# Kernel tuning notes

Hardware: AMD Instinct MI355X
Metric: run time of the kernel (lower is better)

## Reference

```python
import jax, jax.numpy as jnp
import numpy as np

DIM = 1024
HEADS = 8
DIM_HEAD = 64
INNER = HEADS * DIM_HEAD
SCALE = DIM_HEAD ** -0.5


def setup_inputs() -> dict:
    key = jax.random.key(0)
    ks = jax.random.split(key, 6)
    b, n = 2, 2048
    x = jax.random.normal(ks[0], (b, n, DIM), dtype=jnp.float32)
    rel_pos_bias = jax.random.normal(ks[1], (HEADS, n, n), dtype=jnp.float32)
    # learned params (Linear stores W as [out, in]; we keep [in, out] for x @ W)
    Wq = jax.random.normal(ks[2], (DIM, INNER), dtype=jnp.float32) * (DIM ** -0.5)
    Wkv = jax.random.normal(ks[3], (DIM, 2 * DIM_HEAD), dtype=jnp.float32) * (DIM ** -0.5)
    Wo = jax.random.normal(ks[4], (INNER, DIM), dtype=jnp.float32) * (INNER ** -0.5)
    bo = jax.random.normal(ks[5], (DIM,), dtype=jnp.float32) * 0.01
    return {"x": x, "rel_pos_bias": rel_pos_bias, "Wq": Wq, "Wkv": Wkv, "Wo": Wo, "bo": bo}


def reference(x, rel_pos_bias, Wq, Wkv, Wo, bo):
    b, n, _ = x.shape
    q = x @ Wq                       # [b, n, h*d]
    kv = x @ Wkv                     # [b, n, 2d] (multi-query: single shared kv head)
    k, v = kv[..., :DIM_HEAD], kv[..., DIM_HEAD:]
    q = q.reshape(b, n, HEADS, DIM_HEAD).transpose(0, 2, 1, 3) * SCALE  # [b, h, n, d]
    sim = jnp.einsum('bhid,bjd->bhij', q, k)
    sim = sim + rel_pos_bias         # bias broadcast over batch
    causal_mask = jnp.triu(jnp.ones((n, n), dtype=bool), k=1)
    neg = -jnp.finfo(sim.dtype).max
    sim = jnp.where(causal_mask, neg, sim)
    attn = jax.nn.softmax(sim, axis=-1)  # stable softmax (max-subtract internally)
    out = jnp.einsum('bhij,bjd->bhid', attn, v)
    out = out.transpose(0, 2, 1, 3).reshape(b, n, INNER)  # [b, n, h*d]
    return out @ Wo + bo
```

## Files before the change

kernel.cpp:

```cpp
#include <hip/hip_runtime.h>

#define NSEQ 2048
#define NB 2
#define NH 8
#define HD 64
#define DMODEL 1024
#define DINNER 512

#define SLOT_F 4224
#define LOG2E 1.44269504f

typedef __attribute__((ext_vector_type(8))) short bf16x8;
typedef __attribute__((ext_vector_type(4))) float f32x4;

__device__ __forceinline__ ushort f2bf(float f) {
  uint u = __float_as_uint(f);
  uint r = (u + 0x7fffu + ((u >> 16) & 1u)) >> 16;
  return (ushort)r;
}

__device__ __forceinline__ void gld16(const ushort* g, ushort* l) {
  __builtin_amdgcn_global_load_lds(
      (const __attribute__((address_space(1))) uint*)g,
      (__attribute__((address_space(3))) uint*)l, 16, 0, 0);
}

__global__ __launch_bounds__(256) void cast_x_kernel(
    const float* __restrict__ x, ushort* __restrict__ xb) {
  size_t i = ((size_t)blockIdx.x * 256 + threadIdx.x) * 8;
  float4 a = *(const float4*)(x + i);
  float4 b = *(const float4*)(x + i + 4);
  ushort4 o1, o2;
  o1.x = f2bf(a.x); o1.y = f2bf(a.y); o1.z = f2bf(a.z); o1.w = f2bf(a.w);
  o2.x = f2bf(b.x); o2.y = f2bf(b.y); o2.z = f2bf(b.z); o2.w = f2bf(b.w);
  *(ushort4*)(xb + i) = o1;
  *(ushort4*)(xb + i + 4) = o2;
}

__global__ __launch_bounds__(256) void transpose_cast_kernel(
    const float* __restrict__ srcA, const float* __restrict__ srcB,
    int ldA, int ldB, int nsplit, int Ktot, ushort* __restrict__ dst) {
  __shared__ float t[64][65];
  const int k0 = blockIdx.x * 64;
  const int n0 = blockIdx.y * 64;
  const float* src; int ld, nb;
  if (n0 < nsplit) { src = srcA; ld = ldA; nb = n0; }
  else { src = srcB; ld = ldB; nb = n0 - nsplit; }
  const int r = threadIdx.x >> 4;
  const int c = (threadIdx.x & 15) * 4;
#pragma unroll
  for (int rr = r; rr < 64; rr += 16) {
    float4 v = *(const float4*)(src + (size_t)(k0 + rr) * ld + nb + c);
    t[rr][c + 0] = v.x; t[rr][c + 1] = v.y; t[rr][c + 2] = v.z; t[rr][c + 3] = v.w;
  }
  __syncthreads();
#pragma unroll
  for (int rr = r; rr < 64; rr += 16) {
    ushort4 o;
    o.x = f2bf(t[c + 0][rr]); o.y = f2bf(t[c + 1][rr]);
    o.z = f2bf(t[c + 2][rr]); o.w = f2bf(t[c + 3][rr]);
    *(ushort4*)(dst + (size_t)(n0 + rr) * Ktot + k0 + c) = o;
  }
}

__device__ __forceinline__ void stage_tile(const ushort* __restrict__ src, int ld,
                                           int row0, int k0, ushort* lds, int tid) {
#pragma unroll
  for (int i = 0; i < 4; ++i) {
    const int cix = i * 256 + tid;
    const int row = cix >> 3, j = cix & 7;
    uint4 v = *(const uint4*)(src + (size_t)(row0 + row) * ld + k0 + j * 8);
    *(uint4*)((char*)lds + row * 128 + ((j ^ (row & 7)) << 4)) = v;
  }
}

__device__ __forceinline__ void gemm_tile(const ushort* __restrict__ A,
                                          const ushort* __restrict__ Bt, int K,
                                          int m0, int n0, ushort* As, ushort* Bs,
                                          int tid, f32x4 acc[4][4]) {
  const int lane = tid & 63;
  const int w = tid >> 6;
  const int wr = w >> 1, wc = w & 1;
  const int lr = lane & 15, lg = lane >> 4;
  for (int k0 = 0; k0 < K; k0 += 64) {
    __syncthreads();
    stage_tile(A, K, m0, k0, As, tid);
    stage_tile(Bt, K, n0, k0, Bs, tid);
    __syncthreads();
#pragma unroll
    for (int kk = 0; kk < 2; ++kk) {
      bf16x8 af[4], bfr[4];
#pragma unroll
      for (int mi = 0; mi < 4; ++mi) {
        const int r = wr * 64 + mi * 16 + lr;
        af[mi] = *(const bf16x8*)((char*)As + r * 128 + (((kk * 4 + lg) ^ (r & 7)) << 4));
      }
#pragma unroll
      for (int ni = 0; ni < 4; ++ni) {
        const int r = wc * 64 + ni * 16 + lr;
        bfr[ni] = *(const bf16x8*)((char*)Bs + r * 128 + (((kk * 4 + lg) ^ (r & 7)) << 4));
      }
#pragma unroll
      for (int mi = 0; mi < 4; ++mi)
#pragma unroll
        for (int ni = 0; ni < 4; ++ni)
          acc[mi][ni] = __builtin_amdgcn_mfma_f32_16x16x32_bf16(af[mi], bfr[ni],
                                                                acc[mi][ni], 0, 0, 0);
    }
  }
}

__global__ __launch_bounds__(256) void qkv_mfma_kernel(
    const ushort* __restrict__ xb, const ushort* __restrict__ WT1,
    ushort* __restrict__ qb, ushort* __restrict__ ksw, ushort* __restrict__ vsw) {
  __shared__ ushort As[128 * 64];
  __shared__ ushort Bs[128 * 64];
  const int tid = threadIdx.x;
  const int m0 = blockIdx.x * 128, n0 = blockIdx.y * 128;
  f32x4 acc[4][4];
#pragma unroll
  for (int a = 0; a < 4; ++a)
#pragma unroll
    for (int b = 0; b < 4; ++b) acc[a][b] = (f32x4){0.f, 0.f, 0.f, 0.f};
  gemm_tile(xb, WT1, DMODEL, m0, n0, As, Bs, tid, acc);
  const int lane = tid & 63;
  const int w = tid >> 6;
  const int wr = w >> 1, wc = w & 1;
  const int lr = lane & 15, lg = lane >> 4;
#pragma unroll
  for (int mi = 0; mi < 4; ++mi)
#pragma unroll
    for (int ni = 0; ni < 4; ++ni) {
      const int n = n0 + wc * 64 + ni * 16 + lr;
      if (n >= 640) continue;
#pragma unroll
      for (int r = 0; r < 4; ++r) {
        const int m = m0 + wr * 64 + mi * 16 + lg * 4 + r;
        const int bb = m >> 11, key = m & (NSEQ - 1);
        const float v = acc[mi][ni][r];
        if (n < DINNER) {
          const int h = n >> 6, d = n & 63;
          qb[((size_t)((bb * NH + h) * NSEQ) + key) * HD + d] =
              f2bf(v * (0.125f * LOG2E));
        } else if (n < DINNER + HD) {
          const int d = n - DINNER;
          const int t = key >> 6, row = key & 63;
          const int ch = d >> 3, pos = d & 7;
          ksw[(size_t)((bb * 32 + t) * 64 + row) * 64 +
              ((ch ^ (row & 7)) << 3) + pos] = f2bf(v);
        } else {
          const int d = n - DINNER - HD;
          const int pr = key >> 7, kk = key & 127;
          const int ch = kk >> 3, pos = kk & 7;
          vsw[(size_t)((bb * 16 + pr) * 64 + d) * 128 +
              ((ch ^ (d & 15)) << 3) + pos] = f2bf(v);
        }
      }
    }
}

__global__ __launch_bounds__(256) void out_mfma_kernel(
    const ushort* __restrict__ ab, const ushort* __restrict__ WoT,
    const float* __restrict__ bo, float* __restrict__ out) {
  __shared__ ushort As[128 * 64];
  __shared__ ushort Bs[128 * 64];
  const int tid = threadIdx.x;
  const int m0 = blockIdx.x * 128, n0 = blockIdx.y * 128;
  f32x4 acc[4][4];
#pragma unroll
  for (int a = 0; a < 4; ++a)
#pragma unroll
    for (int b = 0; b < 4; ++b) acc[a][b] = (f32x4){0.f, 0.f, 0.f, 0.f};
  gemm_tile(ab, WoT, DINNER, m0, n0, As, Bs, tid, acc);
  const int lane = tid & 63;
  const int w = tid >> 6;
  const int wr = w >> 1, wc = w & 1;
  const int lr = lane & 15, lg = lane >> 4;
#pragma unroll
  for (int mi = 0; mi < 4; ++mi)
#pragma unroll
    for (int ni = 0; ni < 4; ++ni) {
      const int n = n0 + wc * 64 + ni * 16 + lr;
      const float bias = bo[n];
#pragma unroll
      for (int r = 0; r < 4; ++r) {
        const int m = m0 + wr * 64 + mi * 16 + lg * 4 + r;
        out[(size_t)m * DMODEL + n] = acc[mi][ni][r] + bias;
      }
    }
}

__global__ __launch_bounds__(256) void attn_mfma_kernel(
    const ushort* __restrict__ qb, const ushort* __restrict__ ksw,
    const ushort* __restrict__ vsw, const float* __restrict__ rpb,
    ushort* __restrict__ ob, float* __restrict__ scratch) {
  __shared__ ushort Ks[2 * 128 * 64];
  __shared__ ushort Vs[2 * 64 * 128];
  __shared__ ushort Ps[4 * 16 * 128];
  const int tid = threadIdx.x;
  const int lane = tid & 63;
  const int w = tid >> 6;
  const int id = blockIdx.x;
  const int bh = id & 15;
  int qt, p0, p1, partial, ch;
  if (id < 256) {
    qt = 16 + (id >> 4); ch = 0; p0 = 0; p1 = 8; partial = 1;
  } else if (id < 512) {
    qt = 31 - ((id - 256) >> 4); ch = 1; p0 = 8; p1 = (qt >> 1) + 1; partial = 1;
  } else {
    qt = 15 - ((id - 512) >> 4); ch = 0; p0 = 0; p1 = (qt >> 1) + 1; partial = 0;
  }
  const int bb = bh >> 3, h = bh & 7;
  const int q0 = qt * 64;
  const int lr = lane & 15;
  const int lg = lane >> 4;
  const int pdiag = qt >> 1;
  const int qg = q0 + w * 16 + lr;

  const ushort* kpair = ksw + (size_t)bb * 32 * 64 * 64;
  const ushort* vpair = vsw + (size_t)bb * 16 * 64 * 128;
  const ushort* ksrcw = kpair + w * 2048 + lane * 8;
  const ushort* vsrcw = vpair + w * 2048 + lane * 8;
  ushort* kdstw = Ks + w * 2048;
  ushort* vdstw = Vs + w * 2048;

#define ISSUE(pp, bsel)                                                     \
  {                                                                         \
    const ushort* _ks = ksrcw + (size_t)(pp) * 8192;                        \
    const ushort* _vs = vsrcw + (size_t)(pp) * 8192;                        \
    ushort* _kd = kdstw + (bsel) * 8192;                                    \
    ushort* _vd = vdstw + (bsel) * 8192;                                    \
    gld16(_ks + 0 * 512, _kd + 0 * 512);                                    \
    gld16(_ks + 1 * 512, _kd + 1 * 512);                                    \
    gld16(_ks + 2 * 512, _kd + 2 * 512);                                    \
    gld16(_ks + 3 * 512, _kd + 3 * 512);                                    \
    gld16(_vs + 0 * 512, _vd + 0 * 512);                                    \
    gld16(_vs + 1 * 512, _vd + 1 * 512);                                    \
    gld16(_vs + 2 * 512, _vd + 2 * 512);                                    \
    gld16(_vs + 3 * 512, _vd + 3 * 512);                                    \
  }

#define LOAD_BIAS(pp, dst)                                                  \
  {                                                                         \
    const float* _br = rpb + (size_t)h * NSEQ * NSEQ +                      \
                       (size_t)qg * NSEQ + (pp) * 128 + lg * 4;             \
    _Pragma("unroll")                                                       \
    for (int _ct = 0; _ct < 8; ++_ct)                                       \
      dst[_ct] = *(const f32x4*)(_br + _ct * 16);                           \
  }

  bf16x8 qf[2];
  {
    const ushort* qrow = qb + ((size_t)(bh * NSEQ) + qg) * HD + lg * 8;
    qf[0] = *(const bf16x8*)qrow;
    qf[1] = *(const bf16x8*)(qrow + 32);
  }
  f32x4 oaccT[4];
#pragma unroll
  for (int dt = 0; dt < 4; ++dt) oaccT[dt] = (f32x4){0.f, 0.f, 0.f, 0.f};
  float m_run = -1e30f, l_run = 0.f;

  f32x4 bias_c[8], bias_n[8];

  ISSUE(p0, 0);
  LOAD_BIAS(p0, bias_c);
  ISSUE(p0 + 1, 1);
  int curb = 0;

  for (int p = p0; p < p1; ++p) {
    if (p < p1 - 1) {
      asm volatile("s_waitcnt vmcnt(16)" ::: "memory");
    } else {
      asm volatile("s_waitcnt vmcnt(8)" ::: "memory");
    }
    __builtin_amdgcn_sched_barrier(0);
    __builtin_amdgcn_s_barrier();

    const char* Kc = (const char*)(Ks + curb * 8192);
    const char* Vc = (const char*)(Vs + curb * 8192);
    f32x4 s[8];
    __builtin_amdgcn_s_setprio(1);
#pragma unroll
    for (int ct = 0; ct < 8; ++ct) {
      s[ct] = (f32x4){0.f, 0.f, 0.f, 0.f};
      const int krow = ct * 16 + lr;
#pragma unroll
      for (int kk = 0; kk < 2; ++kk) {
        bf16x8 kf = *(const bf16x8*)(Kc + krow * 128 +
                                     (((kk * 4 + lg) ^ (krow & 7)) << 4));
        s[ct] = __builtin_amdgcn_mfma_f32_16x16x32_bf16(kf, qf[kk], s[ct], 0, 0, 0);
      }
    }
    __builtin_amdgcn_s_setprio(0);
    if (p + 1 < p1) LOAD_BIAS(p + 1, bias_n);
#pragma unroll
    for (int ct = 0; ct < 8; ++ct)
#pragma unroll
      for (int r = 0; r < 4; ++r)
        s[ct][r] = fmaf(bias_c[ct][r], LOG2E, s[ct][r]);
    if (p == pdiag) {
#pragma unroll
      for (int ct = 0; ct < 8; ++ct) {
        const int kg = p * 128 + ct * 16 + lg * 4;
#pragma unroll
        for (int r = 0; r < 4; ++r)
          if (kg + r > qg) s[ct][r] = -1e30f;
      }
    }
    float cm[8];
#pragma unroll
    for (int ct = 0; ct < 8; ++ct)
      cm[ct] = fmaxf(fmaxf(s[ct][0], s[ct][1]), fmaxf(s[ct][2], s[ct][3]));
    float mt = fmaxf(fmaxf(fmaxf(cm[0], cm[1]), fmaxf(cm[2], cm[3])),
                     fmaxf(fmaxf(cm[4], cm[5]), fmaxf(cm[6], cm[7])));
    mt = fmaxf(mt, __shfl_xor(mt, 16, 64));
    mt = fmaxf(mt, __shfl_xor(mt, 32, 64));
    const float m_new = fmaxf(m_run, mt);
    const float fac = exp2f(m_run - m_new);
    m_run = m_new;
    float cs[8];
#pragma unroll
    for (int ct = 0; ct < 8; ++ct) {
#pragma unroll
      for (int r = 0; r < 4; ++r) s[ct][r] = exp2f(s[ct][r] - m_new);
      cs[ct] = (s[ct][0] + s[ct][1]) + (s[ct][2] + s[ct][3]);
    }
    float ls = ((cs[0] + cs[1]) + (cs[2] + cs[3])) +
               ((cs[4] + cs[5]) + (cs[6] + cs[7]));
    ls += __shfl_xor(ls, 16, 64);
    ls += __shfl_xor(ls, 32, 64);
    l_run = l_run * fac + ls;
#pragma unroll
    for (int dt = 0; dt < 4; ++dt) oaccT[dt] *= fac;
    char* Pw = (char*)Ps + w * 4096;
#pragma unroll
    for (int ct = 0; ct < 8; ++ct) {
      uint u01, u23;
      asm("v_cvt_pk_bf16_f32 %0, %1, %2" : "=v"(u01) : "v"(s[ct][0]), "v"(s[ct][1]));
      asm("v_cvt_pk_bf16_f32 %0, %1, %2" : "=v"(u23) : "v"(s[ct][2]), "v"(s[ct][3]));
      const int chunk = 2 * ct + (lg >> 1);
      uint2 uv; uv.x = u01; uv.y = u23;
      *(uint2*)(Pw + lr * 256 + (((chunk ^ lr) << 4) | ((lg & 1) * 8))) = uv;
    }
    __builtin_amdgcn_s_setprio(1);
#pragma unroll
    for (int kk = 0; kk < 4; ++kk) {
      bf16x8 pf = *(const bf16x8*)(Pw + lr * 256 + (((kk * 4 + lg) ^ lr) << 4));
#pragma unroll
      for (int dt = 0; dt < 4; ++dt) {
        const int vrow = dt * 16 + lr;
        bf16x8 vf = *(const bf16x8*)(Vc + vrow * 256 +
                                     (((kk * 4 + lg) ^ (vrow & 15)) << 4));
        oaccT[dt] =
            __builtin_amdgcn_mfma_f32_16x16x32_bf16(vf, pf, oaccT[dt], 0, 0, 0);
      }
    }
    __builtin_amdgcn_s_setprio(0);
    __builtin_amdgcn_sched_barrier(0);
    __builtin_amdgcn_s_barrier();
    if (p + 2 < p1) ISSUE(p + 2, curb);
    if (p + 1 < p1) {
#pragma unroll
      for (int ct = 0; ct < 8; ++ct) bias_c[ct] = bias_n[ct];
    }
    curb ^= 1;
  }
#undef ISSUE
#undef LOAD_BIAS
  if (!partial) {
    const float inv = 1.0f / l_run;
    ushort* dst = ob + ((size_t)(bb * NSEQ) + qg) * DINNER + h * HD;
#pragma unroll
    for (int dt = 0; dt < 4; ++dt) {
      uint u01, u23;
      const float o0 = oaccT[dt][0] * inv, o1 = oaccT[dt][1] * inv;
      const float o2 = oaccT[dt][2] * inv, o3 = oaccT[dt][3] * inv;
      asm("v_cvt_pk_bf16_f32 %0, %1, %2" : "=v"(u01) : "v"(o0), "v"(o1));
      asm("v_cvt_pk_bf16_f32 %0, %1, %2" : "=v"(u23) : "v"(o2), "v"(o3));
      uint2 uv; uv.x = u01; uv.y = u23;
      *(uint2*)(dst + dt * 16 + lg * 4) = uv;
    }
  } else {
    float* slot = scratch + (size_t)((bh * 16 + (qt - 16)) * 2 + ch) * SLOT_F;
    const int row = w * 16 + lr;
#pragma unroll
    for (int dt = 0; dt < 4; ++dt)
      *(f32x4*)(slot + row * 64 + dt * 16 + lg * 4) = oaccT[dt];
    if (lg == 0) {
      slot[4096 + row] = m_run;
      slot[4160 + row] = l_run;
    }
  }
}

__global__ __launch_bounds__(256) void attn_merge_kernel(
    const float* __restrict__ scratch, ushort* __restrict__ ob) {
  const int bid = blockIdx.x;
  const int bh = bid >> 4;
  const int qt = 16 + (bid & 15);
  const int bb = bh >> 3, h = bh & 7;
  const float* s0 = scratch + (size_t)((bh * 16 + (qt - 16)) * 2) * SLOT_F;
  const float* s1 = s0 + SLOT_F;
  const int t = threadIdx.x;
  const int r = t >> 2;
  const int c0 = (t & 3) * 16;
  const float m0 = s0[4096 + r], m1 = s1[4096 + r];
  const float M = fmaxf(m0, m1);
  const float sc0 = exp2f(m0 - M), sc1 = exp2f(m1 - M);
  const float L = s0[4160 + r] * sc0 + s1[4160 + r] * sc1;
  const float inv = 1.0f / L;
  ushort* dst = ob + ((size_t)(bb * NSEQ) + qt * 64 + r) * DINNER + h * HD + c0;
#pragma unroll
  for (int j4 = 0; j4 < 4; ++j4) {
    float4 a = *(const float4*)(s0 + r * 64 + c0 + j4 * 4);
    float4 b = *(const float4*)(s1 + r * 64 + c0 + j4 * 4);
    dst[j4 * 4 + 0] = f2bf((a.x * sc0 + b.x * sc1) * inv);
    dst[j4 * 4 + 1] = f2bf((a.y * sc0 + b.y * sc1) * inv);
    dst[j4 * 4 + 2] = f2bf((a.z * sc0 + b.z * sc1) * inv);
    dst[j4 * 4 + 3] = f2bf((a.w * sc0 + b.w * sc1) * inv);
  }
}

extern "C" void kernel_launch(void* const* d_in, const int* in_sizes, int n_in,
                              void* d_out, int out_size, void* d_ws, size_t ws_size,
                              hipStream_t stream) {
  (void)in_sizes; (void)n_in; (void)out_size; (void)ws_size;
  const float* x = (const float*)d_in[0];
  const float* rpb = (const float*)d_in[1];
  const float* Wq = (const float*)d_in[2];
  const float* Wkv = (const float*)d_in[3];
  const float* Wo = (const float*)d_in[4];
  const float* bo = (const float*)d_in[5];
  float* out = (float*)d_out;

  ushort* qbb = (ushort*)d_ws;
  ushort* ksw = qbb + (size_t)NB * NH * NSEQ * HD;
  ushort* vsw = ksw + (size_t)NB * NSEQ * HD;
  ushort* obuf = vsw + (size_t)NB * NSEQ * HD;
  ushort* xb = obuf + (size_t)NB * NSEQ * DINNER;
  ushort* WT1 = xb + (size_t)NB * NSEQ * DMODEL;
  ushort* WoT = WT1 + (size_t)640 * DMODEL;
  float* scratch = (float*)(WoT + (size_t)DMODEL * DINNER);

  cast_x_kernel<<<dim3(2048), 256, 0, stream>>>(x, xb);
  transpose_cast_kernel<<<dim3(16, 10), 256, 0, stream>>>(Wq, Wkv, 512, 128, 512,
                                                          DMODEL, WT1);
  transpose_cast_kernel<<<dim3(8, 16), 256, 0, stream>>>(Wo, Wo, DMODEL, DMODEL,
                                                         DMODEL, DINNER, WoT);
  qkv_mfma_kernel<<<dim3(32, 5), 256, 0, stream>>>(xb, WT1, qbb, ksw, vsw);
  attn_mfma_kernel<<<dim3(768), 256, 0, stream>>>(qbb, ksw, vsw, rpb, obuf,
                                                  scratch);
  attn_merge_kernel<<<dim3(256), 256, 0, stream>>>(scratch, obuf);
  out_mfma_kernel<<<dim3(32, 8), 256, 0, stream>>>(obuf, WoT, bo, out);
}
```

Before: 98.97 us.

## Split attention into single-wave blocks with finer key chunks and direct global K/V reads

New measurement: 163.1 us. +64.8%, slower.

```diff
diff --git a/kernel.cpp b/kernel.cpp
--- a/kernel.cpp
+++ b/kernel.cpp
@@ -7,7 +7,7 @@
 #define DMODEL 1024
 #define DINNER 512
 
-#define SLOT_F 4224
+#define SLOT_F 1056
 #define LOG2E 1.44269504f
 
 typedef __attribute__((ext_vector_type(8))) short bf16x8;
@@ -19,10 +19,10 @@
   return (ushort)r;
 }
 
-__device__ __forceinline__ void gld16(const ushort* g, ushort* l) {
-  __builtin_amdgcn_global_load_lds(
-      (const __attribute__((address_space(1))) uint*)g,
-      (__attribute__((address_space(3))) uint*)l, 16, 0, 0);
+__device__ __forceinline__ int soff(int s, int c) {
+  if (s < 64) return (s - 32) * 2 + c;
+  if (s < 96) return 64 + (s - 64) * 3 + c;
+  return 160 + (s - 96) * 4 + c;
 }
 
 __global__ __launch_bounds__(256) void cast_x_kernel(
@@ -112,7 +112,7 @@
 
 __global__ __launch_bounds__(256) void qkv_mfma_kernel(
     const ushort* __restrict__ xb, const ushort* __restrict__ WT1,
-    ushort* __restrict__ qb, ushort* __restrict__ ksw, ushort* __restrict__ vsw) {
+    ushort* __restrict__ qb, ushort* __restrict__ kb, ushort* __restrict__ vt) {
   __shared__ ushort As[128 * 64];
   __shared__ ushort Bs[128 * 64];
   const int tid = threadIdx.x;
@@ -143,17 +143,9 @@
           qb[((size_t)((bb * NH + h) * NSEQ) + key) * HD + d] =
               f2bf(v * (0.125f * LOG2E));
         } else if (n < DINNER + HD) {
-          const int d = n - DINNER;
-          const int t = key >> 6, row = key & 63;
-          const int ch = d >> 3, pos = d & 7;
-          ksw[(size_t)((bb * 32 + t) * 64 + row) * 64 +
-              ((ch ^ (row & 7)) << 3) + pos] = f2bf(v);
+          kb[((size_t)(bb * NSEQ) + key) * HD + (n - DINNER)] = f2bf(v);
         } else {
-          const int d = n - DINNER - HD;
-          const int pr = key >> 7, kk = key & 127;
-          const int ch = kk >> 3, pos = kk & 7;
-          vsw[(size_t)((bb * 16 + pr) * 64 + d) * 128 +
-              ((ch ^ (d & 15)) << 3) + pos] = f2bf(v);
+          vt[((size_t)(bb * HD) + (n - DINNER - HD)) * NSEQ + key] = f2bf(v);
         }
       }
     }
@@ -190,64 +182,31 @@
     }
 }
 
-__global__ __launch_bounds__(256) void attn_mfma_kernel(
-    const ushort* __restrict__ qb, const ushort* __restrict__ ksw,
-    const ushort* __restrict__ vsw, const float* __restrict__ rpb,
+__global__ __launch_bounds__(64, 3) void attn_mfma_kernel(
+    const ushort* __restrict__ qb, const ushort* __restrict__ kb,
+    const ushort* __restrict__ vt, const float* __restrict__ rpb,
     ushort* __restrict__ ob, float* __restrict__ scratch) {
-  __shared__ ushort Ks[2 * 128 * 64];
-  __shared__ ushort Vs[2 * 64 * 128];
-  __shared__ ushort Ps[4 * 16 * 128];
-  const int tid = threadIdx.x;
-  const int lane = tid & 63;
-  const int w = tid >> 6;
+  __shared__ ushort Ps[16 * 128];
+  const int lane = threadIdx.x;
+  const int lr = lane & 15;
+  const int lg = lane >> 4;
   const int id = blockIdx.x;
   const int bh = id & 15;
-  int qt, p0, p1, partial, ch;
-  if (id < 256) {
-    qt = 16 + (id >> 4); ch = 0; p0 = 0; p1 = 8; partial = 1;
-  } else if (id < 512) {
-    qt = 31 - ((id - 256) >> 4); ch = 1; p0 = 8; p1 = (qt >> 1) + 1; partial = 1;
-  } else {
-    qt = 15 - ((id - 512) >> 4); ch = 0; p0 = 0; p1 = (qt >> 1) + 1; partial = 0;
-  }
+  const int t = 319 - (id >> 4);
+  int s, c;
+  if (t < 32)       { s = t;                      c = 0; }
+  else if (t < 96)  { int u = t - 32;  s = 32 + (u >> 1); c = u & 1; }
+  else if (t < 192) { int u = t - 96;  s = 64 + u / 3;    c = u % 3; }
+  else              { int u = t - 192; s = 96 + (u >> 2); c = u & 3; }
   const int bb = bh >> 3, h = bh & 7;
-  const int q0 = qt * 64;
-  const int lr = lane & 15;
-  const int lg = lane >> 4;
-  const int pdiag = qt >> 1;
-  const int qg = q0 + w * 16 + lr;
-
-  const ushort* kpair = ksw + (size_t)bb * 32 * 64 * 64;
-  const ushort* vpair = vsw + (size_t)bb * 16 * 64 * 128;
-  const ushort* ksrcw = kpair + w * 2048 + lane * 8;
-  const ushort* vsrcw = vpair + w * 2048 + lane * 8;
-  ushort* kdstw = Ks + w * 2048;
-  ushort* vdstw = Vs + w * 2048;
-
-#define ISSUE(pp, bsel)                                                     \
-  {                                                                         \
-    const ushort* _ks = ksrcw + (size_t)(pp) * 8192;                        \
-    const ushort* _vs = vsrcw + (size_t)(pp) * 8192;                        \
-    ushort* _kd = kdstw + (bsel) * 8192;                                    \
-    ushort* _vd = vdstw + (bsel) * 8192;                                    \
-    gld16(_ks + 0 * 512, _kd + 0 * 512);                                    \
-    gld16(_ks + 1 * 512, _kd + 1 * 512);                                    \
-    gld16(_ks + 2 * 512, _kd + 2 * 512);                                    \
-    gld16(_ks + 3 * 512, _kd + 3 * 512);                                    \
-    gld16(_vs + 0 * 512, _vd + 0 * 512);                                    \
-    gld16(_vs + 1 * 512, _vd + 1 * 512);                                    \
-    gld16(_vs + 2 * 512, _vd + 2 * 512);                                    \
-    gld16(_vs + 3 * 512, _vd + 3 * 512);                                    \
-  }
-
-#define LOAD_BIAS(pp, dst)                                                  \
-  {                                                                         \
-    const float* _br = rpb + (size_t)h * NSEQ * NSEQ +                      \
-                       (size_t)qg * NSEQ + (pp) * 128 + lg * 4;             \
-    _Pragma("unroll")                                                       \
-    for (int _ct = 0; _ct < 8; ++_ct)                                       \
-      dst[_ct] = *(const f32x4*)(_br + _ct * 16);                           \
-  }
+  const int pdiag = s >> 3;
+  const int p0 = c * 4;
+  const int p1 = min(p0 + 4, pdiag + 1);
+  const int nch = (pdiag + 4) >> 2;
+  const int qg = s * 16 + lr;
+
+  const ushort* kbase = kb + (size_t)bb * NSEQ * HD;
+  const ushort* vbase = vt + (size_t)bb * HD * NSEQ;
 
   bf16x8 qf[2];
   {
@@ -260,57 +219,46 @@
   for (int dt = 0; dt < 4; ++dt) oaccT[dt] = (f32x4){0.f, 0.f, 0.f, 0.f};
   float m_run = -1e30f, l_run = 0.f;
 
-  f32x4 bias_c[8], bias_n[8];
-
-  ISSUE(p0, 0);
-  LOAD_BIAS(p0, bias_c);
-  ISSUE(p0 + 1, 1);
-  int curb = 0;
-
   for (int p = p0; p < p1; ++p) {
-    if (p < p1 - 1) {
-      asm volatile("s_waitcnt vmcnt(16)" ::: "memory");
-    } else {
-      asm volatile("s_waitcnt vmcnt(8)" ::: "memory");
-    }
-    __builtin_amdgcn_sched_barrier(0);
-    __builtin_amdgcn_s_barrier();
-
-    const char* Kc = (const char*)(Ks + curb * 8192);
-    const char* Vc = (const char*)(Vs + curb * 8192);
-    f32x4 s[8];
+    const int key0 = p * 128;
+    f32x4 bias[8];
+    {
+      const float* br =
+          rpb + (size_t)h * NSEQ * NSEQ + (size_t)qg * NSEQ + key0 + lg * 4;
+#pragma unroll
+      for (int ct = 0; ct < 8; ++ct) bias[ct] = *(const f32x4*)(br + ct * 16);
+    }
+    f32x4 sv[8];
     __builtin_amdgcn_s_setprio(1);
 #pragma unroll
     for (int ct = 0; ct < 8; ++ct) {
-      s[ct] = (f32x4){0.f, 0.f, 0.f, 0.f};
-      const int krow = ct * 16 + lr;
-#pragma unroll
-      for (int kk = 0; kk < 2; ++kk) {
-        bf16x8 kf = *(const bf16x8*)(Kc + krow * 128 +
-                                     (((kk * 4 + lg) ^ (krow & 7)) << 4));
-        s[ct] = __builtin_amdgcn_mfma_f32_16x16x32_bf16(kf, qf[kk], s[ct], 0, 0, 0);
-      }
+      const ushort* krow =
+          kbase + (size_t)(key0 + ct * 16 + lr) * HD + lg * 8;
+      bf16x8 kf0 = *(const bf16x8*)krow;
+      bf16x8 kf1 = *(const bf16x8*)(krow + 32);
+      sv[ct] = (f32x4){0.f, 0.f, 0.f, 0.f};
+      sv[ct] = __builtin_amdgcn_mfma_f32_16x16x32_bf16(kf0, qf[0], sv[ct], 0, 0, 0);
+      sv[ct] = __builtin_amdgcn_mfma_f32_16x16x32_bf16(kf1, qf[1], sv[ct], 0, 0, 0);
     }
     __builtin_amdgcn_s_setprio(0);
-    if (p + 1 < p1) LOAD_BIAS(p + 1, bias_n);
 #pragma unroll
     for (int ct = 0; ct < 8; ++ct)
 #pragma unroll
       for (int r = 0; r < 4; ++r)
-        s[ct][r] = fmaf(bias_c[ct][r], LOG2E, s[ct][r]);
+        sv[ct][r] = fmaf(bias[ct][r], LOG2E, sv[ct][r]);
     if (p == pdiag) {
 #pragma unroll
       for (int ct = 0; ct < 8; ++ct) {
-        const int kg = p * 128 + ct * 16 + lg * 4;
+        const int kg = key0 + ct * 16 + lg * 4;
 #pragma unroll
         for (int r = 0; r < 4; ++r)
-          if (kg + r > qg) s[ct][r] = -1e30f;
+          if (kg + r > qg) sv[ct][r] = -1e30f;
       }
     }
     float cm[8];
 #pragma unroll
     for (int ct = 0; ct < 8; ++ct)
-      cm[ct] = fmaxf(fmaxf(s[ct][0], s[ct][1]), fmaxf(s[ct][2], s[ct][3]));
+      cm[ct] = fmaxf(fmaxf(sv[ct][0], sv[ct][1]), fmaxf(sv[ct][2], sv[ct][3]));
     float mt = fmaxf(fmaxf(fmaxf(cm[0], cm[1]), fmaxf(cm[2], cm[3])),
                      fmaxf(fmaxf(cm[4], cm[5]), fmaxf(cm[6], cm[7])));
     mt = fmaxf(mt, __shfl_xor(mt, 16, 64));
@@ -322,8 +270,8 @@
 #pragma unroll
     for (int ct = 0; ct < 8; ++ct) {
 #pragma unroll
-      for (int r = 0; r < 4; ++r) s[ct][r] = exp2f(s[ct][r] - m_new);
-      cs[ct] = (s[ct][0] + s[ct][1]) + (s[ct][2] + s[ct][3]);
+      for (int r = 0; r < 4; ++r) sv[ct][r] = exp2f(sv[ct][r] - m_new);
+      cs[ct] = (sv[ct][0] + sv[ct][1]) + (sv[ct][2] + sv[ct][3]);
     }
     float ls = ((cs[0] + cs[1]) + (cs[2] + cs[3])) +
                ((cs[4] + cs[5]) + (cs[6] + cs[7]));
@@ -332,12 +280,12 @@
     l_run = l_run * fac + ls;
 #pragma unroll
     for (int dt = 0; dt < 4; ++dt) oaccT[dt] *= fac;
-    char* Pw = (char*)Ps + w * 4096;
+    char* Pw = (char*)Ps;
 #pragma unroll
     for (int ct = 0; ct < 8; ++ct) {
       uint u01, u23;
-      asm("v_cvt_pk_bf16_f32 %0, %1, %2" : "=v"(u01) : "v"(s[ct][0]), "v"(s[ct][1]));
-      asm("v_cvt_pk_bf16_f32 %0, %1, %2" : "=v"(u23) : "v"(s[ct][2]), "v"(s[ct][3]));
+      asm("v_cvt_pk_bf16_f32 %0, %1, %2" : "=v"(u01) : "v"(sv[ct][0]), "v"(sv[ct][1]));
+      asm("v_cvt_pk_bf16_f32 %0, %1, %2" : "=v"(u23) : "v"(sv[ct][2]), "v"(sv[ct][3]));
       const int chunk = 2 * ct + (lg >> 1);
       uint2 uv; uv.x = u01; uv.y = u23;
       *(uint2*)(Pw + lr * 256 + (((chunk ^ lr) << 4) | ((lg & 1) * 8))) = uv;
@@ -348,26 +296,16 @@
       bf16x8 pf = *(const bf16x8*)(Pw + lr * 256 + (((kk * 4 + lg) ^ lr) << 4));
 #pragma unroll
       for (int dt = 0; dt < 4; ++dt) {
-        const int vrow = dt * 16 + lr;
-        bf16x8 vf = *(const bf16x8*)(Vc + vrow * 256 +
-                                     (((kk * 4 + lg) ^ (vrow & 15)) << 4));
+        const ushort* vrow =
+            vbase + (size_t)(dt * 16 + lr) * NSEQ + key0 + kk * 32 + lg * 8;
+        bf16x8 vf = *(const bf16x8*)vrow;
         oaccT[dt] =
             __builtin_amdgcn_mfma_f32_16x16x32_bf16(vf, pf, oaccT[dt], 0, 0, 0);
       }
     }
     __builtin_amdgcn_s_setprio(0);
-    __builtin_amdgcn_sched_barrier(0);
-    __builtin_amdgcn_s_barrier();
-    if (p + 2 < p1) ISSUE(p + 2, curb);
-    if (p + 1 < p1) {
-#pragma unroll
-      for (int ct = 0; ct < 8; ++ct) bias_c[ct] = bias_n[ct];
-    }
-    curb ^= 1;
-  }
-#undef ISSUE
-#undef LOAD_BIAS
-  if (!partial) {
+  }
+  if (nch == 1) {
     const float inv = 1.0f / l_run;
     ushort* dst = ob + ((size_t)(bb * NSEQ) + qg) * DINNER + h * HD;
 #pragma unroll
@@ -381,44 +319,58 @@
       *(uint2*)(dst + dt * 16 + lg * 4) = uv;
     }
   } else {
-    float* slot = scratch + (size_t)((bh * 16 + (qt - 16)) * 2 + ch) * SLOT_F;
-    const int row = w * 16 + lr;
+    float* slot = scratch + ((size_t)(bh * 288) + soff(s, c)) * SLOT_F;
 #pragma unroll
     for (int dt = 0; dt < 4; ++dt)
-      *(f32x4*)(slot + row * 64 + dt * 16 + lg * 4) = oaccT[dt];
+      *(f32x4*)(slot + lr * 64 + dt * 16 + lg * 4) = oaccT[dt];
     if (lg == 0) {
-      slot[4096 + row] = m_run;
-      slot[4160 + row] = l_run;
-    }
-  }
-}
-
-__global__ __launch_bounds__(256) void attn_merge_kernel(
+      slot[1024 + lr] = m_run;
+      slot[1040 + lr] = l_run;
+    }
+  }
+}
+
+__global__ __launch_bounds__(64) void attn_merge_kernel(
     const float* __restrict__ scratch, ushort* __restrict__ ob) {
   const int bid = blockIdx.x;
-  const int bh = bid >> 4;
-  const int qt = 16 + (bid & 15);
+  const int bh = bid / 96;
+  const int s = 32 + bid % 96;
+  const int nch = ((s >> 3) + 4) >> 2;
   const int bb = bh >> 3, h = bh & 7;
-  const float* s0 = scratch + (size_t)((bh * 16 + (qt - 16)) * 2) * SLOT_F;
-  const float* s1 = s0 + SLOT_F;
+  const float* base = scratch + ((size_t)(bh * 288) + soff(s, 0)) * SLOT_F;
   const int t = threadIdx.x;
   const int r = t >> 2;
   const int c0 = (t & 3) * 16;
-  const float m0 = s0[4096 + r], m1 = s1[4096 + r];
-  const float M = fmaxf(m0, m1);
-  const float sc0 = exp2f(m0 - M), sc1 = exp2f(m1 - M);
-  const float L = s0[4160 + r] * sc0 + s1[4160 + r] * sc1;
+  float ms[4], M = -1e30f;
+  for (int ch = 0; ch < nch; ++ch) {
+    ms[ch] = base[(size_t)ch * SLOT_F + 1024 + r];
+    M = fmaxf(M, ms[ch]);
+  }
+  float L = 0.f, sc[4];
+  for (int ch = 0; ch < nch; ++ch) {
+    sc[ch] = exp2f(ms[ch] - M);
+    L += base[(size_t)ch * SLOT_F + 1040 + r] * sc[ch];
+  }
   const float inv = 1.0f / L;
-  ushort* dst = ob + ((size_t)(bb * NSEQ) + qt * 64 + r) * DINNER + h * HD + c0;
-#pragma unroll
-  for (int j4 = 0; j4 < 4; ++j4) {
-    float4 a = *(const float4*)(s0 + r * 64 + c0 + j4 * 4);
-    float4 b = *(const float4*)(s1 + r * 64 + c0 + j4 * 4);
-    dst[j4 * 4 + 0] = f2bf((a.x * sc0 + b.x * sc1) * inv);
-    dst[j4 * 4 + 1] = f2bf((a.y * sc0 + b.y * sc1) * inv);
-    dst[j4 * 4 + 2] = f2bf((a.z * sc0 + b.z * sc1) * inv);
-    dst[j4 * 4 + 3] = f2bf((a.w * sc0 + b.w * sc1) * inv);
-  }
+  float o[16];
+#pragma unroll
+  for (int j = 0; j < 16; ++j) o[j] = 0.f;
+  for (int ch = 0; ch < nch; ++ch) {
+    const float* orow = base + (size_t)ch * SLOT_F + r * 64 + c0;
+    const float f = sc[ch];
+#pragma unroll
+    for (int j4 = 0; j4 < 4; ++j4) {
+      float4 v = *(const float4*)(orow + j4 * 4);
+      o[j4 * 4 + 0] += f * v.x;
+      o[j4 * 4 + 1] += f * v.y;
+      o[j4 * 4 + 2] += f * v.z;
+      o[j4 * 4 + 3] += f * v.w;
+    }
+  }
+  ushort* dst =
+      ob + ((size_t)(bb * NSEQ) + s * 16 + r) * DINNER + h * HD + c0;
+#pragma unroll
+  for (int j = 0; j < 16; ++j) dst[j] = f2bf(o[j] * inv);
 }
 
 extern "C" void kernel_launch(void* const* d_in, const int* in_sizes, int n_in,
@@ -434,9 +386,9 @@
   float* out = (float*)d_out;
 
   ushort* qbb = (ushort*)d_ws;
-  ushort* ksw = qbb + (size_t)NB * NH * NSEQ * HD;
-  ushort* vsw = ksw + (size_t)NB * NSEQ * HD;
-  ushort* obuf = vsw + (size_t)NB * NSEQ * HD;
+  ushort* kbb = qbb + (size_t)NB * NH * NSEQ * HD;
+  ushort* vtb = kbb + (size_t)NB * NSEQ * HD;
+  ushort* obuf = vtb + (size_t)NB * NSEQ * HD;
   ushort* xb = obuf + (size_t)NB * NSEQ * DINNER;
   ushort* WT1 = xb + (size_t)NB * NSEQ * DMODEL;
   ushort* WoT = WT1 + (size_t)640 * DMODEL;
@@ -447,9 +399,9 @@
                                                           DMODEL, WT1);
   transpose_cast_kernel<<<dim3(8, 16), 256, 0, stream>>>(Wo, Wo, DMODEL, DMODEL,
                                                          DMODEL, DINNER, WoT);
-  qkv_mfma_kernel<<<dim3(32, 5), 256, 0, stream>>>(xb, WT1, qbb, ksw, vsw);
-  attn_mfma_kernel<<<dim3(768), 256, 0, stream>>>(qbb, ksw, vsw, rpb, obuf,
-                                                  scratch);
-  attn_merge_kernel<<<dim3(256), 256, 0, stream>>>(scratch, obuf);
+  qkv_mfma_kernel<<<dim3(32, 5), 256, 0, stream>>>(xb, WT1, qbb, kbb, vtb);
+  attn_mfma_kernel<<<dim3(16 * 320), 64, 0, stream>>>(qbb, kbb, vtb, rpb, obuf,
+                                                      scratch);
+  attn_merge_kernel<<<dim3(16 * 96), 64, 0, stream>>>(scratch, obuf);
   out_mfma_kernel<<<dim3(32, 8), 256, 0, stream>>>(obuf, WoT, bo, out);
 }
```

## Use 64-wide key tiles and split long query tiles into up to four KV chunks

Applied to the files above, without the earlier changes.

New measurement: 100.4 us. Within noise of the previous version (+1.4%).

```diff
diff --git a/kernel.cpp b/kernel.cpp
--- a/kernel.cpp
+++ b/kernel.cpp
@@ -8,6 +8,7 @@
 #define DINNER 512
 
 #define SLOT_F 4224
+#define SLOTS_PER_BH 72
 #define LOG2E 1.44269504f
 
 typedef __attribute__((ext_vector_type(8))) short bf16x8;
@@ -17,6 +18,12 @@
   uint u = __float_as_uint(f);
   uint r = (u + 0x7fffu + ((u >> 16) & 1u)) >> 16;
   return (ushort)r;
+}
+
+__device__ __forceinline__ int slot_off(int qt) {
+  if (qt < 16) return (qt - 8) * 2;
+  if (qt < 24) return 16 + (qt - 16) * 3;
+  return 40 + (qt - 24) * 4;
 }
 
 __device__ __forceinline__ void gld16(const ushort* g, ushort* l) {
@@ -145,15 +152,13 @@
         } else if (n < DINNER + HD) {
           const int d = n - DINNER;
           const int t = key >> 6, row = key & 63;
-          const int ch = d >> 3, pos = d & 7;
           ksw[(size_t)((bb * 32 + t) * 64 + row) * 64 +
-              ((ch ^ (row & 7)) << 3) + pos] = f2bf(v);
+              (((d >> 3) ^ (row & 7)) << 3) + (d & 7)] = f2bf(v);
         } else {
           const int d = n - DINNER - HD;
-          const int pr = key >> 7, kk = key & 127;
-          const int ch = kk >> 3, pos = kk & 7;
-          vsw[(size_t)((bb * 16 + pr) * 64 + d) * 128 +
-              ((ch ^ (d & 15)) << 3) + pos] = f2bf(v);
+          const int t = key >> 6, kk = key & 63;
+          vsw[(size_t)((bb * 32 + t) * 64 + d) * 64 +
+              (((kk >> 3) ^ (d & 7)) << 3) + (kk & 7)] = f2bf(v);
         }
       }
     }
@@ -194,58 +199,55 @@
     const ushort* __restrict__ qb, const ushort* __restrict__ ksw,
     const ushort* __restrict__ vsw, const float* __restrict__ rpb,
     ushort* __restrict__ ob, float* __restrict__ scratch) {
-  __shared__ ushort Ks[2 * 128 * 64];
-  __shared__ ushort Vs[2 * 64 * 128];
-  __shared__ ushort Ps[4 * 16 * 128];
+  __shared__ ushort Ks[2 * 64 * 64];
+  __shared__ ushort Vs[2 * 64 * 64];
+  __shared__ ushort Ps[4 * 16 * 64];
   const int tid = threadIdx.x;
   const int lane = tid & 63;
   const int w = tid >> 6;
   const int id = blockIdx.x;
   const int bh = id & 15;
-  int qt, p0, p1, partial, ch;
-  if (id < 256) {
-    qt = 16 + (id >> 4); ch = 0; p0 = 0; p1 = 8; partial = 1;
-  } else if (id < 512) {
-    qt = 31 - ((id - 256) >> 4); ch = 1; p0 = 8; p1 = (qt >> 1) + 1; partial = 1;
-  } else {
-    qt = 15 - ((id - 512) >> 4); ch = 0; p0 = 0; p1 = (qt >> 1) + 1; partial = 0;
-  }
+  const int cid = 79 - (id >> 4);
+  int qt, ch;
+  if (cid < 8)       { qt = cid;                    ch = 0; }
+  else if (cid < 24) { qt = 8 + ((cid - 8) >> 1);   ch = (cid - 8) & 1; }
+  else if (cid < 48) { qt = 16 + (cid - 24) / 3;    ch = (cid - 24) % 3; }
+  else               { qt = 24 + ((cid - 48) >> 2); ch = (cid - 48) & 3; }
+  const int t0 = ch * 8;
+  const int t1 = min(t0 + 8, qt + 1);
+  const int nit = t1 - t0;
+  const int partial = (qt >= 8);
   const int bb = bh >> 3, h = bh & 7;
   const int q0 = qt * 64;
   const int lr = lane & 15;
   const int lg = lane >> 4;
-  const int pdiag = qt >> 1;
   const int qg = q0 + w * 16 + lr;
 
-  const ushort* kpair = ksw + (size_t)bb * 32 * 64 * 64;
-  const ushort* vpair = vsw + (size_t)bb * 16 * 64 * 128;
-  const ushort* ksrcw = kpair + w * 2048 + lane * 8;
-  const ushort* vsrcw = vpair + w * 2048 + lane * 8;
-  ushort* kdstw = Ks + w * 2048;
-  ushort* vdstw = Vs + w * 2048;
-
-#define ISSUE(pp, bsel)                                                     \
+  const ushort* kbase = ksw + (size_t)bb * 32 * 4096;
+  const ushort* vbase = vsw + (size_t)bb * 32 * 4096;
+  const ushort* ksrcw = kbase + w * 1024 + lane * 8;
+  const ushort* vsrcw = vbase + w * 1024 + lane * 8;
+  ushort* kdstw = Ks + w * 1024;
+  ushort* vdstw = Vs + w * 1024;
+
+#define ISSUE(tt, bsel)                                                     \
   {                                                                         \
-    const ushort* _ks = ksrcw + (size_t)(pp) * 8192;                        \
-    const ushort* _vs = vsrcw + (size_t)(pp) * 8192;                        \
-    ushort* _kd = kdstw + (bsel) * 8192;                                    \
-    ushort* _vd = vdstw + (bsel) * 8192;                                    \
-    gld16(_ks + 0 * 512, _kd + 0 * 512);                                    \
-    gld16(_ks + 1 * 512, _kd + 1 * 512);                                    \
-    gld16(_ks + 2 * 512, _kd + 2 * 512);                                    \
-    gld16(_ks + 3 * 512, _kd + 3 * 512);                                    \
-    gld16(_vs + 0 * 512, _vd + 0 * 512);                                    \
-    gld16(_vs + 1 * 512, _vd + 1 * 512);                                    \
-    gld16(_vs + 2 * 512, _vd + 2 * 512);                                    \
-    gld16(_vs + 3 * 512, _vd + 3 * 512);                                    \
-  }
-
-#define LOAD_BIAS(pp, dst)                                                  \
+    const ushort* _ks = ksrcw + (size_t)(tt) * 4096;                        \
+    const ushort* _vs = vsrcw + (size_t)(tt) * 4096;                        \
+    ushort* _kd = kdstw + (bsel) * 4096;                                    \
+    ushort* _vd = vdstw + (bsel) * 4096;                                    \
+    gld16(_ks, _kd);                                                        \
+    gld16(_ks + 512, _kd + 512);                                            \
+    gld16(_vs, _vd);                                                        \
+    gld16(_vs + 512, _vd + 512);                                            \
+  }
+
+#define LOAD_BIAS(tt, dst)                                                  \
   {                                                                         \
     const float* _br = rpb + (size_t)h * NSEQ * NSEQ +                      \
-                       (size_t)qg * NSEQ + (pp) * 128 + lg * 4;             \
+                       (size_t)qg * NSEQ + (tt) * 64 + lg * 4;              \
     _Pragma("unroll")                                                       \
-    for (int _ct = 0; _ct < 8; ++_ct)                                       \
+    for (int _ct = 0; _ct < 4; ++_ct)                                       \
       dst[_ct] = *(const f32x4*)(_br + _ct * 16);                           \
   }
 
@@ -260,28 +262,29 @@
   for (int dt = 0; dt < 4; ++dt) oaccT[dt] = (f32x4){0.f, 0.f, 0.f, 0.f};
   float m_run = -1e30f, l_run = 0.f;
 
-  f32x4 bias_c[8], bias_n[8];
-
-  ISSUE(p0, 0);
-  LOAD_BIAS(p0, bias_c);
-  ISSUE(p0 + 1, 1);
+  f32x4 bias_c[4], bias_n[4];
+
+  ISSUE(t0, 0);
+  LOAD_BIAS(t0, bias_c);
+  ISSUE(t0 + 1, 1);
   int curb = 0;
 
-  for (int p = p0; p < p1; ++p) {
-    if (p < p1 - 1) {
-      asm volatile("s_waitcnt vmcnt(16)" ::: "memory");
+  for (int i = 0; i < nit; ++i) {
+    const int jt = t0 + i;
+    if (i < nit - 1) {
+      asm volatile("s_waitcnt vmcnt(8)" ::: "memory");
     } else {
-      asm volatile("s_waitcnt vmcnt(8)" ::: "memory");
+      asm volatile("s_waitcnt vmcnt(4)" ::: "memory");
     }
     __builtin_amdgcn_sched_barrier(0);
     __builtin_amdgcn_s_barrier();
 
-    const char* Kc = (const char*)(Ks + curb * 8192);
-    const char* Vc = (const char*)(Vs + curb * 8192);
-    f32x4 s[8];
+    const char* Kc = (const char*)(Ks + curb * 4096);
+    const char* Vc = (const char*)(Vs + curb * 4096);
+    f32x4 s[4];
     __builtin_amdgcn_s_setprio(1);
 #pragma unroll
-    for (int ct = 0; ct < 8; ++ct) {
+    for (int ct = 0; ct < 4; ++ct) {
       s[ct] = (f32x4){0.f, 0.f, 0.f, 0.f};
       const int krow = ct * 16 + lr;
 #pragma unroll
@@ -292,65 +295,64 @@
       }
     }
     __builtin_amdgcn_s_setprio(0);
-    if (p + 1 < p1) LOAD_BIAS(p + 1, bias_n);
-#pragma unroll
-    for (int ct = 0; ct < 8; ++ct)
+    if (i + 1 < nit) LOAD_BIAS(jt + 1, bias_n);
+#pragma unroll
+    for (int ct = 0; ct < 4; ++ct)
 #pragma unroll
       for (int r = 0; r < 4; ++r)
         s[ct][r] = fmaf(bias_c[ct][r], LOG2E, s[ct][r]);
-    if (p == pdiag) {
-#pragma unroll
-      for (int ct = 0; ct < 8; ++ct) {
-        const int kg = p * 128 + ct * 16 + lg * 4;
+    if (jt == qt) {
+#pragma unroll
+      for (int ct = 0; ct < 4; ++ct) {
+        const int kg = jt * 64 + ct * 16 + lg * 4;
 #pragma unroll
         for (int r = 0; r < 4; ++r)
           if (kg + r > qg) s[ct][r] = -1e30f;
       }
     }
-    float cm[8];
-#pragma unroll
-    for (int ct = 0; ct < 8; ++ct)
+    float cm[4];
+#pragma unroll
+    for (int ct = 0; ct < 4; ++ct)
       cm[ct] = fmaxf(fmaxf(s[ct][0], s[ct][1]), fmaxf(s[ct][2], s[ct][3]));
-    float mt = fmaxf(fmaxf(fmaxf(cm[0], cm[1]), fmaxf(cm[2], cm[3])),
-                     fmaxf(fmaxf(cm[4], cm[5]), fmaxf(cm[6], cm[7])));
+    float mt = fmaxf(fmaxf(cm[0], cm[1]), fmaxf(cm[2], cm[3]));
     mt = fmaxf(mt, __shfl_xor(mt, 16, 64));
     mt = fmaxf(mt, __shfl_xor(mt, 32, 64));
     const float m_new = fmaxf(m_run, mt);
     const float fac = exp2f(m_run - m_new);
     m_run = m_new;
-    float cs[8];
-#pragma unroll
-    for (int ct = 0; ct < 8; ++ct) {
+    float cs[4];
+#pragma unroll
+    for (int ct = 0; ct < 4; ++ct) {
 #pragma unroll
       for (int r = 0; r < 4; ++r) s[ct][r] = exp2f(s[ct][r] - m_new);
       cs[ct] = (s[ct][0] + s[ct][1]) + (s[ct][2] + s[ct][3]);
     }
-    float ls = ((cs[0] + cs[1]) + (cs[2] + cs[3])) +
-               ((cs[4] + cs[5]) + (cs[6] + cs[7]));
+    float ls = (cs[0] + cs[1]) + (cs[2] + cs[3]);
     ls += __shfl_xor(ls, 16, 64);
     ls += __shfl_xor(ls, 32, 64);
     l_run = l_run * fac + ls;
 #pragma unroll
     for (int dt = 0; dt < 4; ++dt) oaccT[dt] *= fac;
-    char* Pw = (char*)Ps + w * 4096;
-#pragma unroll
-    for (int ct = 0; ct < 8; ++ct) {
+    char* Pw = (char*)Ps + w * 2048;
+#pragma unroll
+    for (int ct = 0; ct < 4; ++ct) {
       uint u01, u23;
       asm("v_cvt_pk_bf16_f32 %0, %1, %2" : "=v"(u01) : "v"(s[ct][0]), "v"(s[ct][1]));
       asm("v_cvt_pk_bf16_f32 %0, %1, %2" : "=v"(u23) : "v"(s[ct][2]), "v"(s[ct][3]));
       const int chunk = 2 * ct + (lg >> 1);
       uint2 uv; uv.x = u01; uv.y = u23;
-      *(uint2*)(Pw + lr * 256 + (((chunk ^ lr) << 4) | ((lg & 1) * 8))) = uv;
+      *(uint2*)(Pw + lr * 128 + (((chunk ^ (lr & 7)) << 4) | ((lg & 1) * 8))) = uv;
     }
     __builtin_amdgcn_s_setprio(1);
 #pragma unroll
-    for (int kk = 0; kk < 4; ++kk) {
-      bf16x8 pf = *(const bf16x8*)(Pw + lr * 256 + (((kk * 4 + lg) ^ lr) << 4));
+    for (int kk = 0; kk < 2; ++kk) {
+      bf16x8 pf = *(const bf16x8*)(Pw + lr * 128 +
+                                   (((kk * 4 + lg) ^ (lr & 7)) << 4));
 #pragma unroll
       for (int dt = 0; dt < 4; ++dt) {
         const int vrow = dt * 16 + lr;
-        bf16x8 vf = *(const bf16x8*)(Vc + vrow * 256 +
-                                     (((kk * 4 + lg) ^ (vrow & 15)) << 4));
+        bf16x8 vf = *(const bf16x8*)(Vc + vrow * 128 +
+                                     (((kk * 4 + lg) ^ (vrow & 7)) << 4));
         oaccT[dt] =
             __builtin_amdgcn_mfma_f32_16x16x32_bf16(vf, pf, oaccT[dt], 0, 0, 0);
       }
@@ -358,10 +360,10 @@
     __builtin_amdgcn_s_setprio(0);
     __builtin_amdgcn_sched_barrier(0);
     __builtin_amdgcn_s_barrier();
-    if (p + 2 < p1) ISSUE(p + 2, curb);
-    if (p + 1 < p1) {
-#pragma unroll
-      for (int ct = 0; ct < 8; ++ct) bias_c[ct] = bias_n[ct];
+    if (i + 2 < nit) ISSUE(t0 + i + 2, curb);
+    if (i + 1 < nit) {
+#pragma unroll
+      for (int ct = 0; ct < 4; ++ct) bias_c[ct] = bias_n[ct];
     }
     curb ^= 1;
   }
@@ -381,7 +383,8 @@
       *(uint2*)(dst + dt * 16 + lg * 4) = uv;
     }
   } else {
-    float* slot = scratch + (size_t)((bh * 16 + (qt - 16)) * 2 + ch) * SLOT_F;
+    float* slot =
+        scratch + (size_t)((bh * SLOTS_PER_BH) + slot_off(qt) + ch) * SLOT_F;
     const int row = w * 16 + lr;
 #pragma unroll
     for (int dt = 0; dt < 4; ++dt)
@@ -396,29 +399,45 @@
 __global__ __launch_bounds__(256) void attn_merge_kernel(
     const float* __restrict__ scratch, ushort* __restrict__ ob) {
   const int bid = blockIdx.x;
-  const int bh = bid >> 4;
-  const int qt = 16 + (bid & 15);
+  const int bh = bid / 24;
+  const int qt = 8 + bid % 24;
+  const int nch = (qt >> 3) + 1;
   const int bb = bh >> 3, h = bh & 7;
-  const float* s0 = scratch + (size_t)((bh * 16 + (qt - 16)) * 2) * SLOT_F;
-  const float* s1 = s0 + SLOT_F;
+  const float* base =
+      scratch + (size_t)((bh * SLOTS_PER_BH) + slot_off(qt)) * SLOT_F;
   const int t = threadIdx.x;
   const int r = t >> 2;
   const int c0 = (t & 3) * 16;
-  const float m0 = s0[4096 + r], m1 = s1[4096 + r];
-  const float M = fmaxf(m0, m1);
-  const float sc0 = exp2f(m0 - M), sc1 = exp2f(m1 - M);
-  const float L = s0[4160 + r] * sc0 + s1[4160 + r] * sc1;
+  float ms[4], M = -1e30f;
+  for (int s = 0; s < nch; ++s) {
+    ms[s] = base[(size_t)s * SLOT_F + 4096 + r];
+    M = fmaxf(M, ms[s]);
+  }
+  float L = 0.f, sc[4];
+  for (int s = 0; s < nch; ++s) {
+    sc[s] = exp2f(ms[s] - M);
+    L += base[(size_t)s * SLOT_F + 4160 + r] * sc[s];
+  }
   const float inv = 1.0f / L;
-  ushort* dst = ob + ((size_t)(bb * NSEQ) + qt * 64 + r) * DINNER + h * HD + c0;
-#pragma unroll
-  for (int j4 = 0; j4 < 4; ++j4) {
-    float4 a = *(const float4*)(s0 + r * 64 + c0 + j4 * 4);
-    float4 b = *(const float4*)(s1 + r * 64 + c0 + j4 * 4);
-    dst[j4 * 4 + 0] = f2bf((a.x * sc0 + b.x * sc1) * inv);
-    dst[j4 * 4 + 1] = f2bf((a.y * sc0 + b.y * sc1) * inv);
-    dst[j4 * 4 + 2] = f2bf((a.z * sc0 + b.z * sc1) * inv);
-    dst[j4 * 4 + 3] = f2bf((a.w * sc0 + b.w * sc1) * inv);
-  }
+  float o[16];
+#pragma unroll
+  for (int j = 0; j < 16; ++j) o[j] = 0.f;
+  for (int s = 0; s < nch; ++s) {
+    const float* orow = base + (size_t)s * SLOT_F + r * 64 + c0;
+    const float f = sc[s];
+#pragma unroll
+    for (int j4 = 0; j4 < 4; ++j4) {
+      float4 v = *(const float4*)(orow + j4 * 4);
+      o[j4 * 4 + 0] += f * v.x;
+      o[j4 * 4 + 1] += f * v.y;
+      o[j4 * 4 + 2] += f * v.z;
+      o[j4 * 4 + 3] += f * v.w;
+    }
+  }
+  const int qg = qt * 64 + r;
+  ushort* dst = ob + ((size_t)(bb * NSEQ) + qg) * DINNER + h * HD + c0;
+#pragma unroll
+  for (int j = 0; j < 16; ++j) dst[j] = f2bf(o[j] * inv);
 }
 
 extern "C" void kernel_launch(void* const* d_in, const int* in_sizes, int n_in,
@@ -448,8 +467,8 @@
   transpose_cast_kernel<<<dim3(8, 16), 256, 0, stream>>>(Wo, Wo, DMODEL, DMODEL,
                                                          DMODEL, DINNER, WoT);
   qkv_mfma_kernel<<<dim3(32, 5), 256, 0, stream>>>(xb, WT1, qbb, ksw, vsw);
-  attn_mfma_kernel<<<dim3(768), 256, 0, stream>>>(qbb, ksw, vsw, rpb, obuf,
-                                                  scratch);
-  attn_merge_kernel<<<dim3(256), 256, 0, stream>>>(scratch, obuf);
+  attn_mfma_kernel<<<dim3(1280), 256, 0, stream>>>(qbb, ksw, vsw, rpb, obuf,
+                                                   scratch);
+  attn_merge_kernel<<<dim3(16 * 24), 256, 0, stream>>>(scratch, obuf);
   out_mfma_kernel<<<dim3(32, 8), 256, 0, stream>>>(obuf, WoT, bo, out);
 }
```
